# Kernel tuning notes

Hardware: AMD Instinct MI355X
Metric: run time of the kernel (lower is better)

## Reference

```python
import jax, jax.numpy as jnp
import numpy as np

TOP_K = 3


def setup_inputs() -> dict:
    key = jax.random.key(0)
    k1, k2, k3 = jax.random.split(key, 3)
    bs, nw, ns, nq = 2, 5, 5, 5
    f_dim, f_h, f_w = 64, 21, 21
    n_img = bs * nw * (ns + nq)
    fm = jax.random.normal(k1, (n_img, f_dim, f_h, f_w), dtype=jnp.float32)
    elabel = jax.random.randint(k2, (n_img,), 0, nw)
    glabel = jax.random.randint(k3, (n_img,), 0, nw)
    return {"fm": fm, "elabel": elabel, "glabel": glabel,
            "bs": bs, "nw": nw, "ns": ns, "nq": nq}


def reference(fm, elabel, glabel, bs, nw, ns, nq):
    _, f_dim, f_h, f_w = fm.shape
    # L2-normalize each spatial descriptor along the channel axis
    fm = fm / (jnp.linalg.norm(fm, axis=1, keepdims=True) + 1e-12)
    fm6 = fm.reshape(bs, nw, ns + nq, f_dim, f_h, f_w)
    sup_fm = fm6[:, :, :ns]   # [bs, nw, ns, c, h, w]
    que_fm = fm6[:, :, ns:]   # [bs, nw, nq, c, h, w]
    # queries: [bs, nw*nq, f_h*f_w, f_dim]
    que = que_fm.reshape(bs, nw * nq, f_dim, f_h * f_w).transpose(0, 1, 3, 2)
    # supports: [bs, nw, ns*f_h*f_w, f_dim]
    sup = sup_fm.transpose(0, 1, 2, 4, 5, 3).reshape(bs, nw, ns * f_h * f_w, f_dim)
    # cosine similarity of every query descriptor to every support descriptor
    # sim: [bs, nw*nq, nw, f_h*f_w, ns*f_h*f_w]
    sim = jnp.einsum('bqxc,bwyc->bqwxy', que, sup)
    # per-query-descriptor top-k nearest support descriptors, summed
    vals, _ = jax.lax.top_k(sim, TOP_K)          # [bs, q, nw, x, k]
    pred = vals.sum(axis=(-2, -1))               # [bs, nw*nq, nw]
    el = elabel.reshape(bs, nw, ns + nq)[:, :, ns:].reshape(-1)
    return pred, el
```

## Files before the change

kernel.cpp:

```cpp
#include <hip/hip_runtime.h>
#include <hip/hip_bf16.h>
#include <math.h>

#define BS 2
#define NW 5
#define NS 5
#define NQ 5
#define FDIM 64
#define FH 21
#define FW 21
#define NPOS (FH*FW)
#define NIMG (BS*NW*(NS+NQ))
#define NQIMG 50
#define IMG_ELEMS (FDIM*NPOS)
#define NY (NS*NPOS)
#define QROWS 448
#define SROWS 2208
#define NSLICE 6
#define NT_S 23
#define NBLK 250
#define NBLK_SIM (NBLK*NSLICE)
#define TILE_B 1024

typedef __attribute__((ext_vector_type(4))) int int4v;
typedef __attribute__((ext_vector_type(8))) unsigned short us8;

static __device__ __forceinline__ void gload_lds16(const void* g, void* l) {
    __builtin_amdgcn_global_load_lds((const __attribute__((address_space(1))) void*)g,
                                     (__attribute__((address_space(3))) void*)l, 16, 0, 0);
}

static __device__ __forceinline__ int med3i(int a, int b, int c) {
    int r;
    asm("v_med3_i32 %0, %1, %2, %3" : "=v"(r) : "v"(a), "v"(b), "v"(c));
    return r;
}

#define T3I(d, a0, a1, a2) do { \
    int _n0 = ((d) > (a0)) ? (d) : (a0); \
    int _n1 = med3i((d), (a0), (a1)); \
    int _n2 = med3i((d), (a1), (a2)); \
    (a0) = _n0; (a1) = _n1; (a2) = _n2; } while (0)

#define T3I4(p, i) do { \
    T3I((p)[0], t0[i], t1[i], t2[i]); \
    T3I((p)[1], t0[i], t1[i], t2[i]); \
    T3I((p)[2], t0[i], t1[i], t2[i]); \
    T3I((p)[3], t0[i], t1[i], t2[i]); } while (0)

#define T3F(d, a0, a1, a2) do { \
    float _n0 = fmaxf((d), (a0)); \
    float _n1 = __builtin_amdgcn_fmed3f((d), (a0), (a1)); \
    float _n2 = __builtin_amdgcn_fmed3f((d), (a1), (a2)); \
    (a0) = _n0; (a1) = _n1; (a2) = _n2; } while (0)

__global__ __launch_bounds__(256) void dn4_normalize(const float* __restrict__ fm,
                                                     const int* __restrict__ elabel,
                                                     char* __restrict__ Qn,
                                                     char* __restrict__ Sn,
                                                     float* __restrict__ out) {
    int gid = blockIdx.x * blockDim.x + threadIdx.x;
    if (gid < 50) {
        int bb = gid / 25, rem = gid % 25, wq = rem / 5, qi = rem % 5;
        out[250 + gid] = (float)elabel[(bb * NW + wq) * (NS + NQ) + NS + qi];
    }
    if (gid < 120) {
        int mat = gid / 12, rr = (gid % 12) >> 2, k = gid & 3;
        int4v zv = {0, 0, 0, 0};
        *(int4v*)(Sn + (size_t)mat * (SROWS * FDIM) + (size_t)(NY + rr) * FDIM + k * 16) = zv;
    }
    if (gid >= NIMG * NPOS) return;
    int img = gid / NPOS;
    int pos = gid - img * NPOS;
    const float* src = fm + (size_t)img * IMG_ELEMS + pos;
    float v[FDIM];
    float ss = 0.f;
#pragma unroll
    for (int c = 0; c < FDIM; ++c) {
        float x = src[(size_t)c * NPOS];
        v[c] = x;
        ss += x * x;
    }
    float rn = 127.0f / (sqrtf(ss) + 1e-12f);
    int w[16];
#pragma unroll
    for (int k = 0; k < 16; ++k) {
        int q0 = __float2int_rn(v[4 * k]     * rn);
        int q1 = __float2int_rn(v[4 * k + 1] * rn);
        int q2 = __float2int_rn(v[4 * k + 2] * rn);
        int q3 = __float2int_rn(v[4 * k + 3] * rn);
        w[k] = (q0 & 0xff) | ((q1 & 0xff) << 8) | ((q2 & 0xff) << 16) | (q3 << 24);
    }
    char* dst;
    int i10 = img % 10;
    if (i10 < NS) {
        int bw = img / 10;
        dst = Sn + (size_t)bw * (SROWS * FDIM) + (size_t)(i10 * NPOS + pos) * FDIM;
    } else {
        int qidx = (img / 10) * NQ + (i10 - NS);
        dst = Qn + (size_t)qidx * (QROWS * FDIM) + (size_t)pos * FDIM;
    }
#pragma unroll
    for (int k = 0; k < 4; ++k) {
        int4v t = {w[4 * k], w[4 * k + 1], w[4 * k + 2], w[4 * k + 3]};
        *(int4v*)(dst + 16 * k) = t;
    }
}

__global__ __launch_bounds__(448, 6) void dn4_sim_mfma(const char* __restrict__ Qn,
                                                       const char* __restrict__ Sn,
                                                       float* __restrict__ gtop3) {
    __shared__ __align__(16) char stile[NT_S][TILE_B];

    int orig = blockIdx.x;
    int xcd = orig & 7, idx = orig >> 3;
    int unit = (xcd < 4 ? xcd * 188 : 4 * 188 + (xcd - 4) * 187) + idx;
    int bid = unit / NSLICE, ys = unit % NSLICE;

    int w = bid % NW;
    int q = (bid / NW) % (NW * NQ);
    int b = bid / (NW * NW * NQ);
    int wq = q / NQ, qi = q % NQ;
    int qidx = (b * NW + wq) * NQ + qi;

    const char* qbase = Qn + (size_t)qidx * (QROWS * FDIM);
    const char* sbase = Sn + (size_t)(b * NW + w) * (SROWS * FDIM);

    int t = threadIdx.x;
    int lane = t & 63, xg = t >> 6;
    int lo16 = lane & 15, hi4 = lane >> 4;

    int stg0 = ((lane >> 2) * FDIM) + ((((lane & 3) ^ ((lane >> 3) & 3)) << 4));
    int tbase = ys * NT_S;

    for (int i = xg; i < NT_S; i += 7)
        gload_lds16(sbase + (size_t)(tbase + i) * TILE_B + stg0, &stile[i][0]);

    int4v bq[4];
#pragma unroll
    for (int i = 0; i < 4; ++i) {
        int xt = xg * 4 + i;
        bq[i] = *(const int4v*)(qbase + (size_t)(xt * 16 + lo16) * FDIM + hi4 * 16);
    }

    asm volatile("s_waitcnt vmcnt(0)" ::: "memory");
    __syncthreads();

    int t0[4], t1[4], t2[4];
#pragma unroll
    for (int i = 0; i < 4; ++i) { t0[i] = INT_MIN; t1[i] = INT_MIN; t2[i] = INT_MIN; }

    int4v zc = {0, 0, 0, 0};

    int rd = lo16 * FDIM + ((hi4 ^ ((lo16 >> 1) & 3)) << 4);

    int4v ca = *(const int4v*)(&stile[0][0] + rd);
    for (int tt = 0; tt < NT_S; ++tt) {
        int4v na = ca;
        if (tt + 1 < NT_S) na = *(const int4v*)(&stile[tt + 1][0] + rd);
        int4v pA = __builtin_amdgcn_mfma_i32_16x16x64_i8(ca, bq[0], zc, 0, 0, 0);
        int4v pB = __builtin_amdgcn_mfma_i32_16x16x64_i8(ca, bq[1], zc, 0, 0, 0);
        T3I4(pA, 0);
        int4v pC = __builtin_amdgcn_mfma_i32_16x16x64_i8(ca, bq[2], zc, 0, 0, 0);
        T3I4(pB, 1);
        int4v pD = __builtin_amdgcn_mfma_i32_16x16x64_i8(ca, bq[3], zc, 0, 0, 0);
        T3I4(pC, 2);
        T3I4(pD, 3);
        ca = na;
    }

    const float INV = 1.0f / 16129.0f;
#pragma unroll
    for (int i = 0; i < 4; ++i) {
        int a0 = t0[i], a1 = t1[i], a2 = t2[i];
#pragma unroll
        for (int mk = 16; mk <= 32; mk <<= 1) {
            int c0 = __shfl_xor(a0, mk, 64);
            int c1 = __shfl_xor(a1, mk, 64);
            int c2 = __shfl_xor(a2, mk, 64);
            T3I(c0, a0, a1, a2);
            T3I(c1, a0, a1, a2);
            T3I(c2, a0, a1, a2);
        }
        if (hi4 == 0) {
            int x = (xg * 4 + i) * 16 + lo16;
            float* dst = gtop3 + ((size_t)(bid * QROWS + x) * NSLICE + ys) * 3;
            dst[0] = (float)a0 * INV;
            dst[1] = (float)a1 * INV;
            dst[2] = (float)a2 * INV;
        }
    }
}

__global__ __launch_bounds__(448) void dn4_merge(const float* __restrict__ gtop3,
                                                 float* __restrict__ out) {
    __shared__ float red[7];
    int bid = blockIdx.x;
    int t = threadIdx.x, lane = t & 63, wv = t >> 6;
    const float* p = gtop3 + (size_t)(bid * QROWS + t) * (NSLICE * 3);
    float a0 = p[0], a1 = p[1], a2 = p[2];
#pragma unroll
    for (int j = 3; j < NSLICE * 3; ++j) {
        float d = p[j];
        T3F(d, a0, a1, a2);
    }
    float s = (t < NPOS) ? (a0 + a1 + a2) : 0.f;
#pragma unroll
    for (int off = 32; off >= 1; off >>= 1) s += __shfl_xor(s, off, 64);
    if (lane == 0) red[wv] = s;
    __syncthreads();
    if (t == 0) {
        float tot = 0.f;
#pragma unroll
        for (int i = 0; i < 7; ++i) tot += red[i];
        out[bid] = tot;
    }
}

extern "C" void kernel_launch(void* const* d_in, const int* in_sizes, int n_in,
                              void* d_out, int out_size, void* d_ws, size_t ws_size,
                              hipStream_t stream) {
    const float* fm     = (const float*)d_in[0];
    const int*   elabel = (const int*)d_in[1];
    float* out = (float*)d_out;

    char* Qn = (char*)d_ws;
    char* Sn = Qn + (size_t)NQIMG * QROWS * FDIM;
    float* gtop3 = (float*)(Sn + (size_t)10 * SROWS * FDIM);

    int nthreads = NIMG * NPOS;
    dn4_normalize<<<(nthreads + 255) / 256, 256, 0, stream>>>(fm, elabel, Qn, Sn, out);
    dn4_sim_mfma<<<NBLK_SIM, 448, 0, stream>>>(Qn, Sn, gtop3);
    dn4_merge<<<NBLK, 448, 0, stream>>>(gtop3, out);
}
```

Measured before the change: 50.00 us.

## Rebalance sim kernel to 4 waves x 7 query tiles, 12 support slices, bf16 partials

Splits the support set into 12 slices of 12 tiles instead of 6 of 23, padding the support rows to 2304 and zeroing the extra padding rows. Each block now runs 256 threads (4 waves), and each wave holds 7 query tiles, so every LDS read of a support tile feeds 7 MFMAs instead of 4. Per-slice top-3 partials are stored as bf16 to halve the intermediate traffic read by the merge kernel. The aim is better MFMA-to-LDS ratio and a more even distribution of blocks across XCDs. The trade-offs are more padded work from the extra zero rows and bf16 rounding of the partial sums.

```diff
diff --git a/kernel.cpp b/kernel.cpp
--- a/kernel.cpp
+++ b/kernel.cpp
@@ -1,6 +1,7 @@
 #include <hip/hip_runtime.h>
 #include <hip/hip_bf16.h>
 #include <math.h>
+#include <limits.h>
 
 #define BS 2
 #define NW 5
@@ -15,15 +16,25 @@
 #define IMG_ELEMS (FDIM*NPOS)
 #define NY (NS*NPOS)
 #define QROWS 448
-#define SROWS 2208
-#define NSLICE 6
-#define NT_S 23
+#define SROWS 2304
+#define NSLICE 12
+#define NT_S 12
 #define NBLK 250
 #define NBLK_SIM (NBLK*NSLICE)
 #define TILE_B 1024
 
 typedef __attribute__((ext_vector_type(4))) int int4v;
-typedef __attribute__((ext_vector_type(8))) unsigned short us8;
+
+static __device__ __forceinline__ unsigned short f2bf(float x) {
+    union { float f; unsigned u; } v; v.f = x;
+    unsigned r = v.u + 0x7fffu + ((v.u >> 16) & 1u);
+    return (unsigned short)(r >> 16);
+}
+
+static __device__ __forceinline__ float bf2f(unsigned short u) {
+    union { unsigned u; float f; } v; v.u = ((unsigned)u) << 16;
+    return v.f;
+}
 
 static __device__ __forceinline__ void gload_lds16(const void* g, void* l) {
     __builtin_amdgcn_global_load_lds((const __attribute__((address_space(1))) void*)g,
@@ -64,8 +75,8 @@
         int bb = gid / 25, rem = gid % 25, wq = rem / 5, qi = rem % 5;
         out[250 + gid] = (float)elabel[(bb * NW + wq) * (NS + NQ) + NS + qi];
     }
-    if (gid < 120) {
-        int mat = gid / 12, rr = (gid % 12) >> 2, k = gid & 3;
+    if (gid < 3960) {
+        int mat = gid / 396, rem = gid % 396, rr = rem >> 2, k = rem & 3;
         int4v zv = {0, 0, 0, 0};
         *(int4v*)(Sn + (size_t)mat * (SROWS * FDIM) + (size_t)(NY + rr) * FDIM + k * 16) = zv;
     }
@@ -107,14 +118,13 @@
     }
 }
 
-__global__ __launch_bounds__(448, 6) void dn4_sim_mfma(const char* __restrict__ Qn,
+__global__ __launch_bounds__(256, 8) void dn4_sim_mfma(const char* __restrict__ Qn,
                                                        const char* __restrict__ Sn,
-                                                       float* __restrict__ gtop3) {
+                                                       unsigned short* __restrict__ gtop3) {
     __shared__ __align__(16) char stile[NT_S][TILE_B];
 
     int orig = blockIdx.x;
-    int xcd = orig & 7, idx = orig >> 3;
-    int unit = (xcd < 4 ? xcd * 188 : 4 * 188 + (xcd - 4) * 187) + idx;
+    int unit = (orig & 7) * (NBLK_SIM / 8) + (orig >> 3);
     int bid = unit / NSLICE, ys = unit % NSLICE;
 
     int w = bid % NW;
@@ -127,28 +137,28 @@
     const char* sbase = Sn + (size_t)(b * NW + w) * (SROWS * FDIM);
 
     int t = threadIdx.x;
-    int lane = t & 63, xg = t >> 6;
+    int lane = t & 63, wv = t >> 6;
     int lo16 = lane & 15, hi4 = lane >> 4;
 
     int stg0 = ((lane >> 2) * FDIM) + ((((lane & 3) ^ ((lane >> 3) & 3)) << 4));
     int tbase = ys * NT_S;
 
-    for (int i = xg; i < NT_S; i += 7)
+    for (int i = wv; i < NT_S; i += 4)
         gload_lds16(sbase + (size_t)(tbase + i) * TILE_B + stg0, &stile[i][0]);
 
-    int4v bq[4];
-#pragma unroll
-    for (int i = 0; i < 4; ++i) {
-        int xt = xg * 4 + i;
+    int4v bq[7];
+#pragma unroll
+    for (int i = 0; i < 7; ++i) {
+        int xt = wv * 7 + i;
         bq[i] = *(const int4v*)(qbase + (size_t)(xt * 16 + lo16) * FDIM + hi4 * 16);
     }
 
     asm volatile("s_waitcnt vmcnt(0)" ::: "memory");
     __syncthreads();
 
-    int t0[4], t1[4], t2[4];
-#pragma unroll
-    for (int i = 0; i < 4; ++i) { t0[i] = INT_MIN; t1[i] = INT_MIN; t2[i] = INT_MIN; }
+    int t0[7], t1[7], t2[7];
+#pragma unroll
+    for (int i = 0; i < 7; ++i) { t0[i] = INT_MIN; t1[i] = INT_MIN; t2[i] = INT_MIN; }
 
     int4v zc = {0, 0, 0, 0};
 
@@ -165,13 +175,19 @@
         T3I4(pB, 1);
         int4v pD = __builtin_amdgcn_mfma_i32_16x16x64_i8(ca, bq[3], zc, 0, 0, 0);
         T3I4(pC, 2);
+        int4v pE = __builtin_amdgcn_mfma_i32_16x16x64_i8(ca, bq[4], zc, 0, 0, 0);
         T3I4(pD, 3);
+        int4v pF = __builtin_amdgcn_mfma_i32_16x16x64_i8(ca, bq[5], zc, 0, 0, 0);
+        T3I4(pE, 4);
+        int4v pG = __builtin_amdgcn_mfma_i32_16x16x64_i8(ca, bq[6], zc, 0, 0, 0);
+        T3I4(pF, 5);
+        T3I4(pG, 6);
         ca = na;
     }
 
     const float INV = 1.0f / 16129.0f;
 #pragma unroll
-    for (int i = 0; i < 4; ++i) {
+    for (int i = 0; i < 7; ++i) {
         int a0 = t0[i], a1 = t1[i], a2 = t2[i];
 #pragma unroll
         for (int mk = 16; mk <= 32; mk <<= 1) {
@@ -183,27 +199,31 @@
             T3I(c2, a0, a1, a2);
         }
         if (hi4 == 0) {
-            int x = (xg * 4 + i) * 16 + lo16;
-            float* dst = gtop3 + ((size_t)(bid * QROWS + x) * NSLICE + ys) * 3;
-            dst[0] = (float)a0 * INV;
-            dst[1] = (float)a1 * INV;
-            dst[2] = (float)a2 * INV;
+            int x = (wv * 7 + i) * 16 + lo16;
+            unsigned short* dst = gtop3 + ((size_t)(bid * QROWS + x) * NSLICE + ys) * 3;
+            dst[0] = f2bf((float)a0 * INV);
+            dst[1] = f2bf((float)a1 * INV);
+            dst[2] = f2bf((float)a2 * INV);
         }
     }
 }
 
-__global__ __launch_bounds__(448) void dn4_merge(const float* __restrict__ gtop3,
+__global__ __launch_bounds__(448) void dn4_merge(const unsigned short* __restrict__ gtop3,
                                                  float* __restrict__ out) {
     __shared__ float red[7];
     int bid = blockIdx.x;
     int t = threadIdx.x, lane = t & 63, wv = t >> 6;
-    const float* p = gtop3 + (size_t)(bid * QROWS + t) * (NSLICE * 3);
-    float a0 = p[0], a1 = p[1], a2 = p[2];
-#pragma unroll
-    for (int j = 3; j < NSLICE * 3; ++j) {
-        float d = p[j];
-        T3F(d, a0, a1, a2);
-    }
+    const unsigned* p = (const unsigned*)(gtop3 + (size_t)(bid * QROWS + t) * (NSLICE * 3));
+    float v[36];
+#pragma unroll
+    for (int j = 0; j < 18; ++j) {
+        unsigned u = p[j];
+        v[2 * j]     = bf2f((unsigned short)(u & 0xffffu));
+        v[2 * j + 1] = bf2f((unsigned short)(u >> 16));
+    }
+    float a0 = v[0], a1 = v[1], a2 = v[2];
+#pragma unroll
+    for (int j = 3; j < 36; ++j) T3F(v[j], a0, a1, a2);
     float s = (t < NPOS) ? (a0 + a1 + a2) : 0.f;
 #pragma unroll
     for (int off = 32; off >= 1; off >>= 1) s += __shfl_xor(s, off, 64);
@@ -226,10 +246,10 @@
 
     char* Qn = (char*)d_ws;
     char* Sn = Qn + (size_t)NQIMG * QROWS * FDIM;
-    float* gtop3 = (float*)(Sn + (size_t)10 * SROWS * FDIM);
+    unsigned short* gtop3 = (unsigned short*)(Sn + (size_t)10 * SROWS * FDIM);
 
     int nthreads = NIMG * NPOS;
     dn4_normalize<<<(nthreads + 255) / 256, 256, 0, stream>>>(fm, elabel, Qn, Sn, out);
-    dn4_sim_mfma<<<NBLK_SIM, 448, 0, stream>>>(Qn, Sn, gtop3);
+    dn4_sim_mfma<<<NBLK_SIM, 256, 0, stream>>>(Qn, Sn, gtop3);
     dn4_merge<<<NBLK, 448, 0, stream>>>(gtop3, out);
 }
```

After: 51.31 us. 2.6% more time.
